# Optimization experiments

Measured on AMD Instinct MI355X. Metric: run time of the kernel, lower is better.

The kernel has to match this reference:

```python
import jax, jax.numpy as jnp
import numpy as np

H = 2048          # hidden_size
IM = 1024         # moe_intermediate_size
E = 16            # n_routed_experts
K = 8             # num_experts_per_tok
N_SHARED = 2      # n_shared_experts
IS = IM * N_SHARED  # shared expert intermediate
B, L = 1, 2048
SCALE = 2.5       # routed_scaling_factor
W_INIT = 0.02


def setup_inputs() -> dict:
    key = jax.random.key(0)
    ks = jax.random.split(key, 9)
    return {
        "hidden_states": jax.random.normal(ks[0], (B, L, H), jnp.float32),
        "gate_w": jax.random.normal(ks[1], (E, H), jnp.float32) * W_INIT,
        "Wg": jax.random.normal(ks[2], (E, H, IM), jnp.float32) * W_INIT,
        "Wu": jax.random.normal(ks[3], (E, H, IM), jnp.float32) * W_INIT,
        "Wd": jax.random.normal(ks[4], (E, IM, H), jnp.float32) * W_INIT,
        "sWg": jax.random.normal(ks[5], (H, IS), jnp.float32) * W_INIT,
        "sWu": jax.random.normal(ks[6], (H, IS), jnp.float32) * W_INIT,
        "sWd": jax.random.normal(ks[7], (IS, H), jnp.float32) * W_INIT,
    }


def reference(hidden_states, gate_w, Wg, Wu, Wd, sWg, sWu, sWd):
    orig_shape = hidden_states.shape
    h = hidden_states.reshape(-1, H)                      # [T, H]
    T = h.shape[0]

    # shared expert (SwiGLU MLP)
    shared = (jax.nn.silu(h @ sWg) * (h @ sWu)) @ sWd     # [T, H]

    # sigmoid router + top-k gating
    router_logits = h @ gate_w.T                          # [T, E]
    routing_weights = jax.nn.sigmoid(router_logits)
    topk_w, topk_idx = jax.lax.top_k(routing_weights, K)  # [T, K]
    topk_w = topk_w / (jnp.sum(topk_w, axis=-1, keepdims=True) + 1e-6)
    topk_w = topk_w * SCALE

    # dense [T, E] combine weights (zero for unselected experts)
    comb = jnp.zeros((T, E), h.dtype).at[jnp.arange(T)[:, None], topk_idx].add(topk_w)

    # all-expert SwiGLU MLP (batched over experts), then weighted combine
    g = jnp.einsum("th,ehi->eti", h, Wg)                  # [E, T, IM]
    u = jnp.einsum("th,ehi->eti", h, Wu)
    eo = jnp.einsum("eti,eih->eth", jax.nn.silu(g) * u, Wd)  # [E, T, H]
    routed = jnp.einsum("eth,te->th", eo, comb)           # [T, H]

    return (shared + routed).reshape(orig_shape)
```

## Files before the change

kernel.cpp:

```cpp
#include <hip/hip_runtime.h>
#include <hip/hip_bf16.h>
#include <stdint.h>

#define H_DIM  2048
#define IM_DIM 1024
#define E_NUM  16
#define TOPK   8
#define IS_DIM 2048
#define SCALE_F 2.5f

#define BM 128
#define BN 128
#define BK 32
#define LDSP 40

typedef __attribute__((ext_vector_type(8))) short   short8;
typedef __attribute__((ext_vector_type(8))) __bf16  bf16x8;
typedef __attribute__((ext_vector_type(4))) float   float4v;
typedef unsigned short ushort_t;

#define GLOAD_LDS16(gp, lp) \
    __builtin_amdgcn_global_load_lds((__attribute__((address_space(1))) void*)(gp), \
                                     (__attribute__((address_space(3))) void*)(lp), 16, 0, 0)

static __device__ __forceinline__ ushort_t f2bf(float x) {
    union { float f; uint32_t u; } v; v.f = x;
    uint32_t r = v.u + 0x7fffu + ((v.u >> 16) & 1u);
    return (ushort_t)(r >> 16);
}

__global__ void cast_h_kernel(const float* __restrict__ h, ushort_t* __restrict__ hb, int n4) {
    int i = blockIdx.x * blockDim.x + threadIdx.x;
    if (i < n4) {
        float4 v = ((const float4*)h)[i];
        ushort4 o;
        o.x = f2bf(v.x); o.y = f2bf(v.y); o.z = f2bf(v.z); o.w = f2bf(v.w);
        ((ushort4*)hb)[i] = o;
    }
}

__global__ void router_kernel(const float* __restrict__ h, const float* __restrict__ gw,
                              float* __restrict__ comb, int T) {
    int t = blockIdx.x;
    int l = threadIdx.x;
    const float* hr = h + (size_t)t * H_DIM;
    __shared__ float logits[E_NUM];
    for (int e = 0; e < E_NUM; e++) {
        const float* g = gw + e * H_DIM;
        float p = 0.f;
        #pragma unroll 8
        for (int j = l; j < H_DIM; j += 64) p += hr[j] * g[j];
        #pragma unroll
        for (int off = 32; off > 0; off >>= 1) p += __shfl_down(p, off);
        if (l == 0) logits[e] = p;
    }
    __syncthreads();
    if (l == 0) {
        float sig[E_NUM]; bool sel[E_NUM];
        #pragma unroll
        for (int e = 0; e < E_NUM; e++) { sig[e] = 1.f / (1.f + expf(-logits[e])); sel[e] = false; }
        #pragma unroll
        for (int k = 0; k < TOPK; k++) {
            int bi = 0; float bv = -1.f;
            #pragma unroll
            for (int e = 0; e < E_NUM; e++)
                if (!sel[e] && sig[e] > bv) { bv = sig[e]; bi = e; }
            sel[bi] = true;
        }
        float s = 0.f;
        #pragma unroll
        for (int e = 0; e < E_NUM; e++) if (sel[e]) s += sig[e];
        float inv = SCALE_F / (s + 1e-6f);
        #pragma unroll
        for (int e = 0; e < E_NUM; e++)
            comb[(size_t)t * E_NUM + e] = sel[e] ? sig[e] * inv : 0.f;
    }
}

__global__ __launch_bounds__(256)
void transpose_cvt_kernel(const float* __restrict__ src, ushort_t* __restrict__ dst,
                          int K, int N, size_t sStride, size_t dStride)
{
    __shared__ float tile[64 * 65];
    int z = blockIdx.z;
    const float* S = src + (size_t)z * sStride;
    ushort_t* D = dst + (size_t)z * dStride;
    int k0 = blockIdx.x * 64, n0 = blockIdx.y * 64;
    int tid = threadIdx.x;
    int tr = tid >> 4, tc = (tid & 15) * 4;
    #pragma unroll
    for (int p = 0; p < 4; p++) {
        int r = tr + 16 * p;
        float4 v = *(const float4*)&S[(size_t)(k0 + r) * N + n0 + tc];
        tile[(tc + 0) * 65 + r] = v.x;
        tile[(tc + 1) * 65 + r] = v.y;
        tile[(tc + 2) * 65 + r] = v.z;
        tile[(tc + 3) * 65 + r] = v.w;
    }
    __syncthreads();
    #pragma unroll
    for (int p = 0; p < 4; p++) {
        int n = tr + 16 * p;
        ushort4 o;
        o.x = f2bf(tile[n * 65 + tc + 0]);
        o.y = f2bf(tile[n * 65 + tc + 1]);
        o.z = f2bf(tile[n * 65 + tc + 2]);
        o.w = f2bf(tile[n * 65 + tc + 3]);
        *(ushort4*)&D[(size_t)(n0 + n) * K + k0 + tc] = o;
    }
}


__global__ __launch_bounds__(256, 2)
void gemm1f_kernel(const ushort_t* __restrict__ A, int lda,
                   const ushort_t* __restrict__ Bg0, const ushort_t* __restrict__ Bu0,
                   size_t bSeg,
                   ushort_t* __restrict__ C0, size_t cSeg, int ldc,
                   const float* __restrict__ comb, int Kdim)
{
    __shared__ ushort_t Als[BM * BK];
    __shared__ ushort_t Bgs[BN * BK];
    __shared__ ushort_t Bus[BN * BK];

    int z = blockIdx.z;
    const ushort_t* Bg = Bg0 + (size_t)z * bSeg;
    const ushort_t* Bu = Bu0 + (size_t)z * bSeg;
    ushort_t* C = C0 + (size_t)z * cSeg;
    int t0 = blockIdx.x * BM, n0 = blockIdx.y * BN;
    int tid = threadIdx.x, lane = tid & 63, wid = tid >> 6;
    int wm = (wid & 1) * 64, wn = (wid >> 1) * 64;
    int quad = lane >> 4, l15 = lane & 15;

    int srow = lane >> 2;
    int scol = (lane & 3) * 8;
    int rb = wid * 32;

    float4v accg[4][4], accu[4][4];
    #pragma unroll
    for (int i = 0; i < 4; i++)
        #pragma unroll
        for (int j = 0; j < 4; j++) {
            accg[i][j] = (float4v){0.f, 0.f, 0.f, 0.f};
            accu[i][j] = (float4v){0.f, 0.f, 0.f, 0.f};
        }

    const ushort_t* Ab0  = A  + (size_t)(t0 + rb + srow)      * lda  + scol;
    const ushort_t* Ab1  = A  + (size_t)(t0 + rb + 16 + srow) * lda  + scol;
    const ushort_t* Bgb0 = Bg + (size_t)(n0 + rb + srow)      * Kdim + scol;
    const ushort_t* Bgb1 = Bg + (size_t)(n0 + rb + 16 + srow) * Kdim + scol;
    const ushort_t* Bub0 = Bu + (size_t)(n0 + rb + srow)      * Kdim + scol;
    const ushort_t* Bub1 = Bu + (size_t)(n0 + rb + 16 + srow) * Kdim + scol;
    ushort_t* lA0  = &Als[rb * BK];
    ushort_t* lA1  = &Als[(rb + 16) * BK];
    ushort_t* lBg0 = &Bgs[rb * BK];
    ushort_t* lBg1 = &Bgs[(rb + 16) * BK];
    ushort_t* lBu0 = &Bus[rb * BK];
    ushort_t* lBu1 = &Bus[(rb + 16) * BK];

    for (int k0 = 0; k0 < Kdim; k0 += BK) {
        GLOAD_LDS16(Ab0 + k0,  lA0);
        GLOAD_LDS16(Ab1 + k0,  lA1);
        GLOAD_LDS16(Bgb0 + k0, lBg0);
        GLOAD_LDS16(Bgb1 + k0, lBg1);
        GLOAD_LDS16(Bub0 + k0, lBu0);
        GLOAD_LDS16(Bub1 + k0, lBu1);
        __syncthreads();

        bf16x8 af[4], bg[4], bu[4];
        #pragma unroll
        for (int i = 0; i < 4; i++)
            af[i] = *(const bf16x8*)&Als[(wm + i * 16 + l15) * BK + quad * 8];
        #pragma unroll
        for (int j = 0; j < 4; j++) {
            bg[j] = *(const bf16x8*)&Bgs[(wn + j * 16 + l15) * BK + quad * 8];
            bu[j] = *(const bf16x8*)&Bus[(wn + j * 16 + l15) * BK + quad * 8];
        }
        #pragma unroll
        for (int i = 0; i < 4; i++)
            #pragma unroll
            for (int j = 0; j < 4; j++) {
                accg[i][j] = __builtin_amdgcn_mfma_f32_16x16x32_bf16(af[i], bg[j], accg[i][j], 0, 0, 0);
                accu[i][j] = __builtin_amdgcn_mfma_f32_16x16x32_bf16(af[i], bu[j], accu[i][j], 0, 0, 0);
            }
        __syncthreads();
    }

    #pragma unroll
    for (int i = 0; i < 4; i++) {
        #pragma unroll
        for (int r = 0; r < 4; r++) {
            int t = t0 + wm + i * 16 + quad * 4 + r;
            float sc = comb ? comb[(size_t)t * E_NUM + z] : 1.f;
            #pragma unroll
            for (int j = 0; j < 4; j++) {
                float g = accg[i][j][r], u = accu[i][j][r];
                float sg = g / (1.f + __expf(-g));
                float v = sg * u * sc;
                int c = n0 + wn + j * 16 + l15;
                C[(size_t)t * ldc + c] = f2bf(v);
            }
        }
    }
}

__global__ __launch_bounds__(256, 2)
void gemm2f_kernel(const ushort_t* __restrict__ A0, size_t aSeg, int lda,
                   const ushort_t* __restrict__ B0, size_t bSeg,
                   float* __restrict__ Out, int N,
                   int nsegPerZ, int Kper, int mode)
{
    __shared__ ushort_t Als[BM * BK];
    __shared__ ushort_t Bls[BN * BK];

    int t0 = blockIdx.x * BM, n0 = blockIdx.y * BN;
    int z = blockIdx.z;
    int tid = threadIdx.x, lane = tid & 63, wid = tid >> 6;
    int wm = (wid & 1) * 64, wn = (wid >> 1) * 64;
    int quad = lane >> 4, l15 = lane & 15;

    int srow = lane >> 2;
    int scol = (lane & 3) * 8;
    int rb = wid * 32;

    float4v acc[4][4];
    #pragma unroll
    for (int i = 0; i < 4; i++)
        #pragma unroll
        for (int j = 0; j < 4; j++) acc[i][j] = (float4v){0.f, 0.f, 0.f, 0.f};

    ushort_t* lA0 = &Als[rb * BK];
    ushort_t* lA1 = &Als[(rb + 16) * BK];
    ushort_t* lB0 = &Bls[rb * BK];
    ushort_t* lB1 = &Bls[(rb + 16) * BK];

    for (int s = 0; s < nsegPerZ; s++) {
        int seg = z * nsegPerZ + s;
        const ushort_t* A = A0 + (size_t)seg * aSeg;
        const ushort_t* B = B0 + (size_t)seg * bSeg;
        const ushort_t* Ab0 = A + (size_t)(t0 + rb + srow)      * lda  + scol;
        const ushort_t* Ab1 = A + (size_t)(t0 + rb + 16 + srow) * lda  + scol;
        const ushort_t* Bb0 = B + (size_t)(n0 + rb + srow)      * Kper + scol;
        const ushort_t* Bb1 = B + (size_t)(n0 + rb + 16 + srow) * Kper + scol;

        for (int k0 = 0; k0 < Kper; k0 += BK) {
            GLOAD_LDS16(Ab0 + k0, lA0);
            GLOAD_LDS16(Ab1 + k0, lA1);
            GLOAD_LDS16(Bb0 + k0, lB0);
            GLOAD_LDS16(Bb1 + k0, lB1);
            __syncthreads();

            bf16x8 af[4], bf[4];
            #pragma unroll
            for (int i = 0; i < 4; i++)
                af[i] = *(const bf16x8*)&Als[(wm + i * 16 + l15) * BK + quad * 8];
            #pragma unroll
            for (int j = 0; j < 4; j++)
                bf[j] = *(const bf16x8*)&Bls[(wn + j * 16 + l15) * BK + quad * 8];
            #pragma unroll
            for (int i = 0; i < 4; i++)
                #pragma unroll
                for (int j = 0; j < 4; j++)
                    acc[i][j] = __builtin_amdgcn_mfma_f32_16x16x32_bf16(af[i], bf[j], acc[i][j], 0, 0, 0);
            __syncthreads();
        }
    }

    #pragma unroll
    for (int i = 0; i < 4; i++) {
        #pragma unroll
        for (int r = 0; r < 4; r++) {
            int t = t0 + wm + i * 16 + quad * 4 + r;
            #pragma unroll
            for (int j = 0; j < 4; j++) {
                int c = n0 + wn + j * 16 + l15;
                size_t idx = (size_t)t * N + c;
                float v = acc[i][j][r];
                if (mode == 0) Out[idx] = v;
                else if (mode == 1) Out[idx] += v;
                else atomicAdd(&Out[idx], v);
            }
        }
    }
}


__global__ __launch_bounds__(256)
void gemm1_kernel(const ushort_t* __restrict__ A, int lda,
                  const float* __restrict__ Bg0, const float* __restrict__ Bu0,
                  size_t bSeg, int ldb,
                  ushort_t* __restrict__ C0, size_t cSeg, int ldc,
                  const float* __restrict__ comb, int Kdim)
{
    __shared__ ushort_t Als[BM * LDSP];
    __shared__ ushort_t Bgs[BN * LDSP];
    __shared__ ushort_t Bus[BN * LDSP];

    int z = blockIdx.z;
    const float* Bg = Bg0 + (size_t)z * bSeg;
    const float* Bu = Bu0 + (size_t)z * bSeg;
    ushort_t* C = C0 + (size_t)z * cSeg;

    int t0 = blockIdx.x * BM;
    int n0 = blockIdx.y * BN;
    int tid = threadIdx.x;
    int lane = tid & 63, wid = tid >> 6;
    int wm = (wid & 1) * 64, wn = (wid >> 1) * 64;
    int quad = lane >> 4, l15 = lane & 15;

    float4v accg[4][4], accu[4][4];
    #pragma unroll
    for (int i = 0; i < 4; i++)
        #pragma unroll
        for (int j = 0; j < 4; j++) {
            accg[i][j] = (float4v){0.f, 0.f, 0.f, 0.f};
            accu[i][j] = (float4v){0.f, 0.f, 0.f, 0.f};
        }

    int a_r  = tid >> 2, a_oc = tid & 3;
    int b_ko = (tid >> 4) & 3;
    int b_n  = 2 * ((tid & 15) + ((tid >> 6) << 4));

    for (int k0 = 0; k0 < Kdim; k0 += BK) {
        __syncthreads();
        {
            const ushort_t* s0 = A + (size_t)(t0 + a_r) * lda + k0 + a_oc * 8;
            *(short8*)&Als[a_r * LDSP + a_oc * 8] = *(const short8*)s0;
            const ushort_t* s1 = A + (size_t)(t0 + a_r + 64) * lda + k0 + a_oc * 8;
            *(short8*)&Als[(a_r + 64) * LDSP + a_oc * 8] = *(const short8*)s1;
        }
        {
            short8 g0, g1, u0, u1;
            #pragma unroll
            for (int j = 0; j < 8; j++) {
                size_t roff = (size_t)(k0 + b_ko * 8 + j) * ldb + n0 + b_n;
                float2 vg = *(const float2*)&Bg[roff];
                float2 vu = *(const float2*)&Bu[roff];
                g0[j] = (short)f2bf(vg.x); g1[j] = (short)f2bf(vg.y);
                u0[j] = (short)f2bf(vu.x); u1[j] = (short)f2bf(vu.y);
            }
            *(short8*)&Bgs[b_n * LDSP + b_ko * 8]       = g0;
            *(short8*)&Bgs[(b_n + 1) * LDSP + b_ko * 8] = g1;
            *(short8*)&Bus[b_n * LDSP + b_ko * 8]       = u0;
            *(short8*)&Bus[(b_n + 1) * LDSP + b_ko * 8] = u1;
        }
        __syncthreads();

        bf16x8 af[4], bg[4], bu[4];
        #pragma unroll
        for (int i = 0; i < 4; i++)
            af[i] = *(const bf16x8*)&Als[(wm + i * 16 + l15) * LDSP + quad * 8];
        #pragma unroll
        for (int j = 0; j < 4; j++) {
            bg[j] = *(const bf16x8*)&Bgs[(wn + j * 16 + l15) * LDSP + quad * 8];
            bu[j] = *(const bf16x8*)&Bus[(wn + j * 16 + l15) * LDSP + quad * 8];
        }
        #pragma unroll
        for (int i = 0; i < 4; i++)
            #pragma unroll
            for (int j = 0; j < 4; j++) {
                accg[i][j] = __builtin_amdgcn_mfma_f32_16x16x32_bf16(af[i], bg[j], accg[i][j], 0, 0, 0);
                accu[i][j] = __builtin_amdgcn_mfma_f32_16x16x32_bf16(af[i], bu[j], accu[i][j], 0, 0, 0);
            }
    }

    #pragma unroll
// ... 31 lines not shown
    int quad = lane >> 4, l15 = lane & 15;

    float4v acc[4][4];
    #pragma unroll
    for (int i = 0; i < 4; i++)
        #pragma unroll
        for (int j = 0; j < 4; j++) acc[i][j] = (float4v){0.f, 0.f, 0.f, 0.f};

    int a_r  = tid >> 2, a_oc = tid & 3;
    int b_ko = (tid >> 4) & 3;
    int b_n  = 2 * ((tid & 15) + ((tid >> 6) << 4));

    for (int seg = 0; seg < nseg; seg++) {
        const ushort_t* A = A0 + (size_t)seg * aSeg;
        const float*    B = B0 + (size_t)seg * bSeg;
        for (int k0 = 0; k0 < Kper; k0 += BK) {
            __syncthreads();
            {
                const ushort_t* s0 = A + (size_t)(t0 + a_r) * lda + k0 + a_oc * 8;
                *(short8*)&Als[a_r * LDSP + a_oc * 8] = *(const short8*)s0;
                const ushort_t* s1 = A + (size_t)(t0 + a_r + 64) * lda + k0 + a_oc * 8;
                *(short8*)&Als[(a_r + 64) * LDSP + a_oc * 8] = *(const short8*)s1;
            }
            {
                short8 r0, r1;
                #pragma unroll
                for (int j = 0; j < 8; j++) {
                    size_t roff = (size_t)(k0 + b_ko * 8 + j) * ldb + n0 + b_n;
                    float2 v = *(const float2*)&B[roff];
                    r0[j] = (short)f2bf(v.x); r1[j] = (short)f2bf(v.y);
                }
                *(short8*)&Bls[b_n * LDSP + b_ko * 8]       = r0;
                *(short8*)&Bls[(b_n + 1) * LDSP + b_ko * 8] = r1;
            }
            __syncthreads();

            bf16x8 af[4], bf[4];
            #pragma unroll
            for (int i = 0; i < 4; i++)
                af[i] = *(const bf16x8*)&Als[(wm + i * 16 + l15) * LDSP + quad * 8];
            #pragma unroll
            for (int j = 0; j < 4; j++)
                bf[j] = *(const bf16x8*)&Bls[(wn + j * 16 + l15) * LDSP + quad * 8];
            #pragma unroll
            for (int i = 0; i < 4; i++)
                #pragma unroll
                for (int j = 0; j < 4; j++)
                    acc[i][j] = __builtin_amdgcn_mfma_f32_16x16x32_bf16(af[i], bf[j], acc[i][j], 0, 0, 0);
        }
    }

    #pragma unroll
    for (int i = 0; i < 4; i++) {
        #pragma unroll
        for (int r = 0; r < 4; r++) {
            int t = t0 + wm + i * 16 + quad * 4 + r;
            #pragma unroll
            for (int j = 0; j < 4; j++) {
                int c = n0 + wn + j * 16 + l15;
                size_t idx = (size_t)t * N + c;
                float v = acc[i][j][r];
                if (accum) Out[idx] += v; else Out[idx] = v;
            }
        }
    }
}


extern "C" void kernel_launch(void* const* d_in, const int* in_sizes, int n_in,
                              void* d_out, int out_size, void* d_ws, size_t ws_size,
                              hipStream_t stream) {
    const float* h      = (const float*)d_in[0];
    const float* gate_w = (const float*)d_in[1];
    const float* Wg     = (const float*)d_in[2];
    const float* Wu     = (const float*)d_in[3];
    const float* Wd     = (const float*)d_in[4];
    const float* sWg    = (const float*)d_in[5];
    const float* sWu    = (const float*)d_in[6];
    const float* sWd    = (const float*)d_in[7];
    float* out = (float*)d_out;
    int T = in_sizes[0] / H_DIM;
    (void)n_in; (void)out_size;

    char* ws = (char*)d_ws;
    size_t off = 0;
    auto alloc = [&](size_t bytes) -> void* {
        void* p = ws + off;
        off = (off + bytes + 255) & ~(size_t)255;
        return p;
    };
    ushort_t* h_bf  = (ushort_t*)alloc((size_t)T * H_DIM * 2);
    float*    comb  = (float*)   alloc((size_t)T * E_NUM * 4);
    ushort_t* act_s = (ushort_t*)alloc((size_t)T * IS_DIM * 2);
    ushort_t* act_r = (ushort_t*)alloc((size_t)E_NUM * T * IM_DIM * 2);
    ushort_t* bufS1 = (ushort_t*)alloc((size_t)IS_DIM * H_DIM * 2);
    ushort_t* bufS2 = (ushort_t*)alloc((size_t)IS_DIM * H_DIM * 2);
    ushort_t* bufW1 = (ushort_t*)alloc((size_t)E_NUM * IM_DIM * H_DIM * 2);
    ushort_t* bufW2 = (ushort_t*)alloc((size_t)E_NUM * IM_DIM * H_DIM * 2);
    size_t need = off;

    int n4 = T * H_DIM / 4;
    cast_h_kernel<<<(n4 + 255) / 256, 256, 0, stream>>>(h, h_bf, n4);
    router_kernel<<<T, 64, 0, stream>>>(h, gate_w, comb, T);

    if (ws_size >= need) {
        transpose_cvt_kernel<<<dim3(H_DIM / 64, IS_DIM / 64, 1), 256, 0, stream>>>(
            sWg, bufS1, H_DIM, IS_DIM, 0, 0);
        transpose_cvt_kernel<<<dim3(H_DIM / 64, IS_DIM / 64, 1), 256, 0, stream>>>(
            sWu, bufS2, H_DIM, IS_DIM, 0, 0);
        gemm1f_kernel<<<dim3(T / BM, IS_DIM / BN, 1), 256, 0, stream>>>(
            h_bf, H_DIM, bufS1, bufS2, 0, act_s, 0, IS_DIM, nullptr, H_DIM);

        transpose_cvt_kernel<<<dim3(H_DIM / 64, IM_DIM / 64, E_NUM), 256, 0, stream>>>(
            Wg, bufW1, H_DIM, IM_DIM, (size_t)H_DIM * IM_DIM, (size_t)IM_DIM * H_DIM);
        transpose_cvt_kernel<<<dim3(H_DIM / 64, IM_DIM / 64, E_NUM), 256, 0, stream>>>(
            Wu, bufW2, H_DIM, IM_DIM, (size_t)H_DIM * IM_DIM, (size_t)IM_DIM * H_DIM);
        gemm1f_kernel<<<dim3(T / BM, IM_DIM / BN, E_NUM), 256, 0, stream>>>(
            h_bf, H_DIM, bufW1, bufW2, (size_t)IM_DIM * H_DIM,
            act_r, (size_t)T * IM_DIM, IM_DIM, comb, H_DIM);

        transpose_cvt_kernel<<<dim3(IS_DIM / 64, H_DIM / 64, 1), 256, 0, stream>>>(
            sWd, bufS1, IS_DIM, H_DIM, 0, 0);
        gemm2f_kernel<<<dim3(T / BM, H_DIM / BN, 1), 256, 0, stream>>>(
            act_s, 0, IS_DIM, bufS1, 0, out, H_DIM, 1, IS_DIM, 0);

        transpose_cvt_kernel<<<dim3(IM_DIM / 64, H_DIM / 64, E_NUM), 256, 0, stream>>>(
            Wd, bufW1, IM_DIM, H_DIM, (size_t)IM_DIM * H_DIM, (size_t)H_DIM * IM_DIM);
        gemm2f_kernel<<<dim3(T / BM, H_DIM / BN, 2), 256, 0, stream>>>(
            act_r, (size_t)T * IM_DIM, IM_DIM, bufW1, (size_t)H_DIM * IM_DIM,
            out, H_DIM, E_NUM / 2, IM_DIM, 2);
    } else {
        gemm1_kernel<<<dim3(T / BM, IS_DIM / BN, 1), 256, 0, stream>>>(
            h_bf, H_DIM, sWg, sWu, 0, IS_DIM, act_s, 0, IS_DIM, nullptr, H_DIM);
        gemm1_kernel<<<dim3(T / BM, IM_DIM / BN, E_NUM), 256, 0, stream>>>(
            h_bf, H_DIM, Wg, Wu, (size_t)H_DIM * IM_DIM, IM_DIM,
            act_r, (size_t)T * IM_DIM, IM_DIM, comb, H_DIM);
        gemm2_kernel<<<dim3(T / BM, H_DIM / BN, 1), 256, 0, stream>>>(
            act_s, 0, IS_DIM, sWd, 0, H_DIM, out, H_DIM, 1, IS_DIM, 0);
        gemm2_kernel<<<dim3(T / BM, H_DIM / BN, 1), 256, 0, stream>>>(
            act_r, (size_t)T * IM_DIM, IM_DIM, Wd, (size_t)IM_DIM * H_DIM, H_DIM,
            out, H_DIM, E_NUM, IM_DIM, 1);
    }
}
```

Measured before the change: 1.147 ms.

## Rewrite expert GEMMs as double-buffered 512-thread kernels with shared experts as extra segments

Replaces the single-buffered 128x128 GEMM kernels with 256x128-tile, 512-thread kernels. They use double-buffered LDS with a 64-wide K step, XOR-swizzled LDS layout, explicit vmcnt waits and raised MFMA priority, so global loads overlap with compute. The shared expert is split into two IM-wide segments and appended to the routed experts, so one batched launch per GEMM stage covers all 18 segments. The down projection splits segments across 6 z-slices that atomically accumulate into an output zeroed up front. This trades more fp32 atomics and a larger LDS footprint (one block per CU) for fewer launches and better latency hiding.

```diff
diff --git a/kernel.cpp b/kernel.cpp
--- a/kernel.cpp
+++ b/kernel.cpp
@@ -23,10 +23,18 @@
     __builtin_amdgcn_global_load_lds((__attribute__((address_space(1))) void*)(gp), \
                                      (__attribute__((address_space(3))) void*)(lp), 16, 0, 0)
 
+#define BAR()    asm volatile("s_barrier" ::: "memory")
+#define VMCNT(n) asm volatile("s_waitcnt vmcnt(" #n ")" ::: "memory")
+
 static __device__ __forceinline__ ushort_t f2bf(float x) {
     union { float f; uint32_t u; } v; v.f = x;
     uint32_t r = v.u + 0x7fffu + ((v.u >> 16) & 1u);
     return (ushort_t)(r >> 16);
+}
+
+__global__ void zero4_kernel(float4* __restrict__ p, int n4) {
+    int i = blockIdx.x * blockDim.x + threadIdx.x;
+    if (i < n4) p[i] = make_float4(0.f, 0.f, 0.f, 0.f);
 }
 
 __global__ void cast_h_kernel(const float* __restrict__ h, ushort_t* __restrict__ hb, int n4) {
@@ -111,176 +119,280 @@
 }
 
 
-__global__ __launch_bounds__(256, 2)
-void gemm1f_kernel(const ushort_t* __restrict__ A, int lda,
-                   const ushort_t* __restrict__ Bg0, const ushort_t* __restrict__ Bu0,
-                   size_t bSeg,
-                   ushort_t* __restrict__ C0, size_t cSeg, int ldc,
-                   const float* __restrict__ comb, int Kdim)
+__global__ __launch_bounds__(512, 1)
+void gemm1_8p(const ushort_t* __restrict__ A,
+              const ushort_t* __restrict__ G0,
+              const ushort_t* __restrict__ U0,
+              ushort_t* __restrict__ C0,
+              const float* __restrict__ comb, int T)
 {
-    __shared__ ushort_t Als[BM * BK];
-    __shared__ ushort_t Bgs[BN * BK];
-    __shared__ ushort_t Bus[BN * BK];
-
-    int z = blockIdx.z;
-    const ushort_t* Bg = Bg0 + (size_t)z * bSeg;
-    const ushort_t* Bu = Bu0 + (size_t)z * bSeg;
-    ushort_t* C = C0 + (size_t)z * cSeg;
-    int t0 = blockIdx.x * BM, n0 = blockIdx.y * BN;
-    int tid = threadIdx.x, lane = tid & 63, wid = tid >> 6;
-    int wm = (wid & 1) * 64, wn = (wid >> 1) * 64;
-    int quad = lane >> 4, l15 = lane & 15;
-
-    int srow = lane >> 2;
-    int scol = (lane & 3) * 8;
-    int rb = wid * 32;
-
-    float4v accg[4][4], accu[4][4];
-    #pragma unroll
-    for (int i = 0; i < 4; i++)
-        #pragma unroll
-        for (int j = 0; j < 4; j++) {
+    __shared__ ushort_t As[2][256 * 64];
+    __shared__ ushort_t Gs[2][128 * 64];
+    __shared__ ushort_t Us[2][128 * 64];
+
+    const int z   = blockIdx.z;
+    const int t0  = blockIdx.x * 256;
+    const int n0  = blockIdx.y * 128;
+    const int tid = threadIdx.x;
+    const int lane = tid & 63, wid = tid >> 6;
+    const int wm = (wid >> 2) * 128;
+    const int wn = (wid & 3) * 32;
+    const int quad = lane >> 4, l15 = lane & 15;
+    const int sw = l15 & 7;
+
+    const int lrow8 = lane >> 3;
+    const int lslot = (lane & 7) ^ lrow8;
+
+    const ushort_t* G = G0 + (size_t)z * IM_DIM * H_DIM;
+    const ushort_t* U = U0 + (size_t)z * IM_DIM * H_DIM;
+    ushort_t*       C = C0 + (size_t)z * T * IM_DIM;
+
+    const int aq0 = wm + (wid & 3) * 32;
+    const int bq0 = (wid & 3) * 32 + (wid >> 2) * 16;
+    const ushort_t* aG = A + (size_t)(t0 + aq0 + lrow8) * H_DIM + lslot * 8;
+    const ushort_t* gG = G + (size_t)(n0 + bq0 + lrow8) * H_DIM + lslot * 8;
+    const ushort_t* uG = U + (size_t)(n0 + bq0 + lrow8) * H_DIM + lslot * 8;
+
+#define G1_ISSUE_A(bb, ko) do { \
+    GLOAD_LDS16(aG + (ko),               &As[bb][(aq0 + 0) * 64]);  \
+    GLOAD_LDS16(aG + (ko) + 8 * H_DIM,   &As[bb][(aq0 + 8) * 64]);  \
+    GLOAD_LDS16(aG + (ko) + 16 * H_DIM,  &As[bb][(aq0 + 16) * 64]); \
+    GLOAD_LDS16(aG + (ko) + 24 * H_DIM,  &As[bb][(aq0 + 24) * 64]); \
+} while (0)
+#define G1_ISSUE_G(bb, ko) do { \
+    GLOAD_LDS16(gG + (ko),               &Gs[bb][(bq0 + 0) * 64]);  \
+    GLOAD_LDS16(gG + (ko) + 8 * H_DIM,   &Gs[bb][(bq0 + 8) * 64]);  \
+} while (0)
+#define G1_ISSUE_U(bb, ko) do { \
+    GLOAD_LDS16(uG + (ko),               &Us[bb][(bq0 + 0) * 64]);  \
+    GLOAD_LDS16(uG + (ko) + 8 * H_DIM,   &Us[bb][(bq0 + 8) * 64]);  \
+} while (0)
+
+    float4v accg[8][2], accu[8][2];
+    #pragma unroll
+    for (int i = 0; i < 8; ++i)
+        #pragma unroll
+        for (int j = 0; j < 2; ++j) {
             accg[i][j] = (float4v){0.f, 0.f, 0.f, 0.f};
             accu[i][j] = (float4v){0.f, 0.f, 0.f, 0.f};
         }
 
-    const ushort_t* Ab0  = A  + (size_t)(t0 + rb + srow)      * lda  + scol;
-    const ushort_t* Ab1  = A  + (size_t)(t0 + rb + 16 + srow) * lda  + scol;
-    const ushort_t* Bgb0 = Bg + (size_t)(n0 + rb + srow)      * Kdim + scol;
-    const ushort_t* Bgb1 = Bg + (size_t)(n0 + rb + 16 + srow) * Kdim + scol;
-    const ushort_t* Bub0 = Bu + (size_t)(n0 + rb + srow)      * Kdim + scol;
-    const ushort_t* Bub1 = Bu + (size_t)(n0 + rb + 16 + srow) * Kdim + scol;
-    ushort_t* lA0  = &Als[rb * BK];
-    ushort_t* lA1  = &Als[(rb + 16) * BK];
-    ushort_t* lBg0 = &Bgs[rb * BK];
-    ushort_t* lBg1 = &Bgs[(rb + 16) * BK];
-    ushort_t* lBu0 = &Bus[rb * BK];
-    ushort_t* lBu1 = &Bus[(rb + 16) * BK];
-
-    for (int k0 = 0; k0 < Kdim; k0 += BK) {
-        GLOAD_LDS16(Ab0 + k0,  lA0);
-        GLOAD_LDS16(Ab1 + k0,  lA1);
-        GLOAD_LDS16(Bgb0 + k0, lBg0);
-        GLOAD_LDS16(Bgb1 + k0, lBg1);
-        GLOAD_LDS16(Bub0 + k0, lBu0);
-        GLOAD_LDS16(Bub1 + k0, lBu1);
-        __syncthreads();
-
-        bf16x8 af[4], bg[4], bu[4];
-        #pragma unroll
-        for (int i = 0; i < 4; i++)
-            af[i] = *(const bf16x8*)&Als[(wm + i * 16 + l15) * BK + quad * 8];
-        #pragma unroll
-        for (int j = 0; j < 4; j++) {
-            bg[j] = *(const bf16x8*)&Bgs[(wn + j * 16 + l15) * BK + quad * 8];
-            bu[j] = *(const bf16x8*)&Bus[(wn + j * 16 + l15) * BK + quad * 8];
-        }
-        #pragma unroll
-        for (int i = 0; i < 4; i++)
-            #pragma unroll
-            for (int j = 0; j < 4; j++) {
-                accg[i][j] = __builtin_amdgcn_mfma_f32_16x16x32_bf16(af[i], bg[j], accg[i][j], 0, 0, 0);
-                accu[i][j] = __builtin_amdgcn_mfma_f32_16x16x32_bf16(af[i], bu[j], accu[i][j], 0, 0, 0);
+    G1_ISSUE_A(0, 0); G1_ISSUE_G(0, 0); G1_ISSUE_U(0, 0);
+
+    const int NT = H_DIM / 64;
+    for (int t = 0; t < NT; ++t) {
+        const int b  = t & 1;
+        const int ko = (t + 1) * 64;
+        if (t + 1 < NT) {
+            G1_ISSUE_A(b ^ 1, ko);
+            G1_ISSUE_G(b ^ 1, ko);
+            VMCNT(6);
+        } else {
+            VMCNT(0);
+        }
+        BAR();
+
+        bf16x8 a_[4][2], g_[2][2], u_[2][2];
+        #pragma unroll
+        for (int i = 0; i < 4; ++i) {
+            const int r = wm + i * 16 + l15;
+            #pragma unroll
+            for (int kk = 0; kk < 2; ++kk)
+                a_[i][kk] = *(const bf16x8*)&As[b][r * 64 + (((kk * 4 + quad) ^ sw) << 3)];
+        }
+        #pragma unroll
+        for (int j = 0; j < 2; ++j) {
+            const int r = wn + j * 16 + l15;
+            #pragma unroll
+            for (int kk = 0; kk < 2; ++kk)
+                g_[j][kk] = *(const bf16x8*)&Gs[b][r * 64 + (((kk * 4 + quad) ^ sw) << 3)];
+        }
+        __builtin_amdgcn_s_setprio(1);
+        #pragma unroll
+        for (int i = 0; i < 4; ++i)
+            #pragma unroll
+            for (int j = 0; j < 2; ++j)
+                #pragma unroll
+                for (int kk = 0; kk < 2; ++kk)
+                    accg[i][j] = __builtin_amdgcn_mfma_f32_16x16x32_bf16(a_[i][kk], g_[j][kk], accg[i][j], 0, 0, 0);
+        __builtin_amdgcn_s_setprio(0);
+        BAR();
+
+        if (t + 1 < NT) G1_ISSUE_U(b ^ 1, ko);
+        #pragma unroll
+        for (int j = 0; j < 2; ++j) {
+            const int r = wn + j * 16 + l15;
+            #pragma unroll
+            for (int kk = 0; kk < 2; ++kk)
+                u_[j][kk] = *(const bf16x8*)&Us[b][r * 64 + (((kk * 4 + quad) ^ sw) << 3)];
+        }
+        __builtin_amdgcn_s_setprio(1);
+        #pragma unroll
+        for (int i = 0; i < 4; ++i)
+            #pragma unroll
+            for (int j = 0; j < 2; ++j)
+                #pragma unroll
+                for (int kk = 0; kk < 2; ++kk)
+                    accu[i][j] = __builtin_amdgcn_mfma_f32_16x16x32_bf16(a_[i][kk], u_[j][kk], accu[i][j], 0, 0, 0);
+        __builtin_amdgcn_s_setprio(0);
+        BAR();
+
+        #pragma unroll
+        for (int i = 0; i < 4; ++i) {
+            const int r = wm + (i + 4) * 16 + l15;
+            #pragma unroll
+            for (int kk = 0; kk < 2; ++kk)
+                a_[i][kk] = *(const bf16x8*)&As[b][r * 64 + (((kk * 4 + quad) ^ sw) << 3)];
+        }
+        __builtin_amdgcn_s_setprio(1);
+        #pragma unroll
+        for (int i = 0; i < 4; ++i)
+            #pragma unroll
+            for (int j = 0; j < 2; ++j)
+                #pragma unroll
+                for (int kk = 0; kk < 2; ++kk)
+                    accg[i + 4][j] = __builtin_amdgcn_mfma_f32_16x16x32_bf16(a_[i][kk], g_[j][kk], accg[i + 4][j], 0, 0, 0);
+        __builtin_amdgcn_s_setprio(0);
+        BAR();
+
+        __builtin_amdgcn_s_setprio(1);
+        #pragma unroll
+        for (int i = 0; i < 4; ++i)
+            #pragma unroll
+            for (int j = 0; j < 2; ++j)
+                #pragma unroll
+                for (int kk = 0; kk < 2; ++kk)
+                    accu[i + 4][j] = __builtin_amdgcn_mfma_f32_16x16x32_bf16(a_[i][kk], u_[j][kk], accu[i + 4][j], 0, 0, 0);
+        __builtin_amdgcn_s_setprio(0);
+    }
+
+    #pragma unroll
+    for (int i = 0; i < 8; ++i) {
+        #pragma unroll
+        for (int r = 0; r < 4; ++r) {
+            const int tr = t0 + wm + i * 16 + quad * 4 + r;
+            const float sc = (z < E_NUM) ? comb[(size_t)tr * E_NUM + z] : 1.f;
+            #pragma unroll
+            for (int j = 0; j < 2; ++j) {
+                const float g = accg[i][j][r], u = accu[i][j][r];
+                const float v = (g / (1.f + __expf(-g))) * u * sc;
+                C[(size_t)tr * IM_DIM + (n0 + wn + j * 16 + l15)] = f2bf(v);
             }
-        __syncthreads();
-    }
-
-    #pragma unroll
-    for (int i = 0; i < 4; i++) {
-        #pragma unroll
-        for (int r = 0; r < 4; r++) {
-            int t = t0 + wm + i * 16 + quad * 4 + r;
-            float sc = comb ? comb[(size_t)t * E_NUM + z] : 1.f;
-            #pragma unroll
-            for (int j = 0; j < 4; j++) {
-                float g = accg[i][j][r], u = accu[i][j][r];
-                float sg = g / (1.f + __expf(-g));
-                float v = sg * u * sc;
-                int c = n0 + wn + j * 16 + l15;
-                C[(size_t)t * ldc + c] = f2bf(v);
-            }
-        }
-    }
-}
-
-__global__ __launch_bounds__(256, 2)
-void gemm2f_kernel(const ushort_t* __restrict__ A0, size_t aSeg, int lda,
-                   const ushort_t* __restrict__ B0, size_t bSeg,
-                   float* __restrict__ Out, int N,
-                   int nsegPerZ, int Kper, int mode)
+        }
+    }
+#undef G1_ISSUE_A
+#undef G1_ISSUE_G
+#undef G1_ISSUE_U
+}
+
+__global__ __launch_bounds__(512, 1)
+void gemm2_8p(const ushort_t* __restrict__ A0,
+              const ushort_t* __restrict__ B0,
+              float* __restrict__ Out, int T, int nseg)
 {
-    __shared__ ushort_t Als[BM * BK];
-    __shared__ ushort_t Bls[BN * BK];
-
-    int t0 = blockIdx.x * BM, n0 = blockIdx.y * BN;
-    int z = blockIdx.z;
-    int tid = threadIdx.x, lane = tid & 63, wid = tid >> 6;
-    int wm = (wid & 1) * 64, wn = (wid >> 1) * 64;
-    int quad = lane >> 4, l15 = lane & 15;
-
-    int srow = lane >> 2;
-    int scol = (lane & 3) * 8;
-    int rb = wid * 32;
+    __shared__ ushort_t As[2][256 * 64];
+    __shared__ ushort_t Bs[2][128 * 64];
+
+    const int z   = blockIdx.z;
+    const int t0  = blockIdx.x * 256;
+    const int n0  = blockIdx.y * 128;
+    const int tid = threadIdx.x;
+    const int lane = tid & 63, wid = tid >> 6;
+    const int wm = (wid >> 1) * 64;
+    const int wn = (wid & 1) * 64;
+    const int quad = lane >> 4, l15 = lane & 15;
+    const int sw = l15 & 7;
+    const int lrow8 = lane >> 3;
+    const int lslot = (lane & 7) ^ lrow8;
+
+    const int aq0 = (wid >> 1) * 64 + (wid & 1) * 32;
+    const int bq0 = (wid & 1) * 64 + (wid >> 1) * 16;
+    const ushort_t* aG = A0 + (size_t)(t0 + aq0 + lrow8) * IM_DIM + lslot * 8;
+    const ushort_t* bG = B0 + (size_t)(n0 + bq0 + lrow8) * IM_DIM + lslot * 8;
+    const size_t segA = (size_t)T * IM_DIM;
+    const size_t segB = (size_t)H_DIM * IM_DIM;
+
+#define G2_ISSUE(bb, tt) do { \
+    const int    s_  = z * nseg + ((tt) >> 4); \
+    const size_t ao_ = (size_t)s_ * segA + ((tt) & 15) * 64; \
+    const size_t bo_ = (size_t)s_ * segB + ((tt) & 15) * 64; \
+    GLOAD_LDS16(aG + ao_,                &As[bb][(aq0 + 0) * 64]);  \
+    GLOAD_LDS16(aG + ao_ + 8 * IM_DIM,   &As[bb][(aq0 + 8) * 64]);  \
+    GLOAD_LDS16(aG + ao_ + 16 * IM_DIM,  &As[bb][(aq0 + 16) * 64]); \
+    GLOAD_LDS16(aG + ao_ + 24 * IM_DIM,  &As[bb][(aq0 + 24) * 64]); \
+    GLOAD_LDS16(bG + bo_,                &Bs[bb][(bq0 + 0) * 64]);  \
+    GLOAD_LDS16(bG + bo_ + 8 * IM_DIM,   &Bs[bb][(bq0 + 8) * 64]);  \
+} while (0)
 
     float4v acc[4][4];
     #pragma unroll
-    for (int i = 0; i < 4; i++)
-        #pragma unroll
-        for (int j = 0; j < 4; j++) acc[i][j] = (float4v){0.f, 0.f, 0.f, 0.f};
-
-    ushort_t* lA0 = &Als[rb * BK];
-    ushort_t* lA1 = &Als[(rb + 16) * BK];
-    ushort_t* lB0 = &Bls[rb * BK];
-    ushort_t* lB1 = &Bls[(rb + 16) * BK];
-
-    for (int s = 0; s < nsegPerZ; s++) {
-        int seg = z * nsegPerZ + s;
-        const ushort_t* A = A0 + (size_t)seg * aSeg;
-        const ushort_t* B = B0 + (size_t)seg * bSeg;
-        const ushort_t* Ab0 = A + (size_t)(t0 + rb + srow)      * lda  + scol;
-        const ushort_t* Ab1 = A + (size_t)(t0 + rb + 16 + srow) * lda  + scol;
-        const ushort_t* Bb0 = B + (size_t)(n0 + rb + srow)      * Kper + scol;
-        const ushort_t* Bb1 = B + (size_t)(n0 + rb + 16 + srow) * Kper + scol;
-
-        for (int k0 = 0; k0 < Kper; k0 += BK) {
-            GLOAD_LDS16(Ab0 + k0, lA0);
-            GLOAD_LDS16(Ab1 + k0, lA1);
-            GLOAD_LDS16(Bb0 + k0, lB0);
-            GLOAD_LDS16(Bb1 + k0, lB1);
-            __syncthreads();
-
-            bf16x8 af[4], bf[4];
-            #pragma unroll
-            for (int i = 0; i < 4; i++)
-                af[i] = *(const bf16x8*)&Als[(wm + i * 16 + l15) * BK + quad * 8];
-            #pragma unroll
-            for (int j = 0; j < 4; j++)
-                bf[j] = *(const bf16x8*)&Bls[(wn + j * 16 + l15) * BK + quad * 8];
-            #pragma unroll
-            for (int i = 0; i < 4; i++)
-                #pragma unroll
-                for (int j = 0; j < 4; j++)
-                    acc[i][j] = __builtin_amdgcn_mfma_f32_16x16x32_bf16(af[i], bf[j], acc[i][j], 0, 0, 0);
-            __syncthreads();
-        }
-    }
-
-    #pragma unroll
-    for (int i = 0; i < 4; i++) {
-        #pragma unroll
-        for (int r = 0; r < 4; r++) {
-            int t = t0 + wm + i * 16 + quad * 4 + r;
-            #pragma unroll
-            for (int j = 0; j < 4; j++) {
-                int c = n0 + wn + j * 16 + l15;
-                size_t idx = (size_t)t * N + c;
-                float v = acc[i][j][r];
-                if (mode == 0) Out[idx] = v;
-                else if (mode == 1) Out[idx] += v;
-                else atomicAdd(&Out[idx], v);
-            }
-        }
-    }
+    for (int i = 0; i < 4; ++i)
+        #pragma unroll
+        for (int j = 0; j < 4; ++j) acc[i][j] = (float4v){0.f, 0.f, 0.f, 0.f};
+
+    G2_ISSUE(0, 0);
+    const int nTT = nseg * (IM_DIM / 64);
+    for (int tt = 0; tt < nTT; ++tt) {
+        const int b = tt & 1;
+        if (tt + 1 < nTT) { G2_ISSUE(b ^ 1, tt + 1); VMCNT(6); }
+        else              { VMCNT(0); }
+        BAR();
+
+        bf16x8 a_[4][2], b_[4][2];
+        #pragma unroll
+        for (int i = 0; i < 4; ++i) {
+            const int r = wm + i * 16 + l15;
+            #pragma unroll
+            for (int kk = 0; kk < 2; ++kk)
+                a_[i][kk] = *(const bf16x8*)&As[b][r * 64 + (((kk * 4 + quad) ^ sw) << 3)];
+        }
+        #pragma unroll
+        for (int j = 0; j < 2; ++j) {
+            const int r = wn + j * 16 + l15;
+            #pragma unroll
+            for (int kk = 0; kk < 2; ++kk)
+                b_[j][kk] = *(const bf16x8*)&Bs[b][r * 64 + (((kk * 4 + quad) ^ sw) << 3)];
+        }
+        __builtin_amdgcn_s_setprio(1);
+        #pragma unroll
+        for (int i = 0; i < 4; ++i)
+            #pragma unroll
+            for (int j = 0; j < 2; ++j)
+                #pragma unroll
+                for (int kk = 0; kk < 2; ++kk)
+                    acc[i][j] = __builtin_amdgcn_mfma_f32_16x16x32_bf16(a_[i][kk], b_[j][kk], acc[i][j], 0, 0, 0);
+        __builtin_amdgcn_s_setprio(0);
+        BAR();
+
+        #pragma unroll
+        for (int j = 0; j < 2; ++j) {
+            const int r = wn + (j + 2) * 16 + l15;
+            #pragma unroll
+            for (int kk = 0; kk < 2; ++kk)
+                b_[j + 2][kk] = *(const bf16x8*)&Bs[b][r * 64 + (((kk * 4 + quad) ^ sw) << 3)];
+        }
+        __builtin_amdgcn_s_setprio(1);
+        #pragma unroll
+        for (int i = 0; i < 4; ++i)
+            #pragma unroll
+            for (int j = 2; j < 4; ++j)
+                #pragma unroll
+                for (int kk = 0; kk < 2; ++kk)
+                    acc[i][j] = __builtin_amdgcn_mfma_f32_16x16x32_bf16(a_[i][kk], b_[j][kk], acc[i][j], 0, 0, 0);
+        __builtin_amdgcn_s_setprio(0);
+        BAR();
+    }
+
+    #pragma unroll
+    for (int i = 0; i < 4; ++i)
+        #pragma unroll
+        for (int r = 0; r < 4; ++r) {
+            const int tr = t0 + wm + i * 16 + quad * 4 + r;
+            #pragma unroll
+            for (int j = 0; j < 4; ++j)
+                atomicAdd(&Out[(size_t)tr * H_DIM + n0 + wn + j * 16 + l15], acc[i][j][r]);
+        }
+#undef G2_ISSUE
 }
 
 
@@ -478,6 +590,8 @@
     int T = in_sizes[0] / H_DIM;
     (void)n_in; (void)out_size;
 
+    const int NSEG = E_NUM + 2;
+
     char* ws = (char*)d_ws;
     size_t off = 0;
     auto alloc = [&](size_t bytes) -> void* {
@@ -485,14 +599,11 @@
         off = (off + bytes + 255) & ~(size_t)255;
         return p;
     };
-    ushort_t* h_bf  = (ushort_t*)alloc((size_t)T * H_DIM * 2);
-    float*    comb  = (float*)   alloc((size_t)T * E_NUM * 4);
-    ushort_t* act_s = (ushort_t*)alloc((size_t)T * IS_DIM * 2);
-    ushort_t* act_r = (ushort_t*)alloc((size_t)E_NUM * T * IM_DIM * 2);
-    ushort_t* bufS1 = (ushort_t*)alloc((size_t)IS_DIM * H_DIM * 2);
-    ushort_t* bufS2 = (ushort_t*)alloc((size_t)IS_DIM * H_DIM * 2);
-    ushort_t* bufW1 = (ushort_t*)alloc((size_t)E_NUM * IM_DIM * H_DIM * 2);
-    ushort_t* bufW2 = (ushort_t*)alloc((size_t)E_NUM * IM_DIM * H_DIM * 2);
+    ushort_t* h_bf = (ushort_t*)alloc((size_t)T * H_DIM * 2);
+    float*    comb = (float*)   alloc((size_t)T * E_NUM * 4);
+    ushort_t* act  = (ushort_t*)alloc((size_t)NSEG * T * IM_DIM * 2);
+    ushort_t* bufG = (ushort_t*)alloc((size_t)NSEG * IM_DIM * H_DIM * 2);
+    ushort_t* bufU = (ushort_t*)alloc((size_t)NSEG * IM_DIM * H_DIM * 2);
     size_t need = off;
 
     int n4 = T * H_DIM / 4;
@@ -500,32 +611,33 @@
     router_kernel<<<T, 64, 0, stream>>>(h, gate_w, comb, T);
 
     if (ws_size >= need) {
-        transpose_cvt_kernel<<<dim3(H_DIM / 64, IS_DIM / 64, 1), 256, 0, stream>>>(
-            sWg, bufS1, H_DIM, IS_DIM, 0, 0);
-        transpose_cvt_kernel<<<dim3(H_DIM / 64, IS_DIM / 64, 1), 256, 0, stream>>>(
-            sWu, bufS2, H_DIM, IS_DIM, 0, 0);
-        gemm1f_kernel<<<dim3(T / BM, IS_DIM / BN, 1), 256, 0, stream>>>(
-            h_bf, H_DIM, bufS1, bufS2, 0, act_s, 0, IS_DIM, nullptr, H_DIM);
+        zero4_kernel<<<(n4 + 255) / 256, 256, 0, stream>>>((float4*)out, n4);
 
         transpose_cvt_kernel<<<dim3(H_DIM / 64, IM_DIM / 64, E_NUM), 256, 0, stream>>>(
-            Wg, bufW1, H_DIM, IM_DIM, (size_t)H_DIM * IM_DIM, (size_t)IM_DIM * H_DIM);
+            Wg, bufG, H_DIM, IM_DIM, (size_t)H_DIM * IM_DIM, (size_t)IM_DIM * H_DIM);
+        transpose_cvt_kernel<<<dim3(H_DIM / 64, IM_DIM / 64, 2), 256, 0, stream>>>(
+            sWg, bufG + (size_t)E_NUM * IM_DIM * H_DIM, H_DIM, IS_DIM,
+            (size_t)IM_DIM, (size_t)IM_DIM * H_DIM);
         transpose_cvt_kernel<<<dim3(H_DIM / 64, IM_DIM / 64, E_NUM), 256, 0, stream>>>(
-            Wu, bufW2, H_DIM, IM_DIM, (size_t)H_DIM * IM_DIM, (size_t)IM_DIM * H_DIM);
-        gemm1f_kernel<<<dim3(T / BM, IM_DIM / BN, E_NUM), 256, 0, stream>>>(
-            h_bf, H_DIM, bufW1, bufW2, (size_t)IM_DIM * H_DIM,
-            act_r, (size_t)T * IM_DIM, IM_DIM, comb, H_DIM);
-
-        transpose_cvt_kernel<<<dim3(IS_DIM / 64, H_DIM / 64, 1), 256, 0, stream>>>(
-            sWd, bufS1, IS_DIM, H_DIM, 0, 0);
-        gemm2f_kernel<<<dim3(T / BM, H_DIM / BN, 1), 256, 0, stream>>>(
-            act_s, 0, IS_DIM, bufS1, 0, out, H_DIM, 1, IS_DIM, 0);
+            Wu, bufU, H_DIM, IM_DIM, (size_t)H_DIM * IM_DIM, (size_t)IM_DIM * H_DIM);
+        transpose_cvt_kernel<<<dim3(H_DIM / 64, IM_DIM / 64, 2), 256, 0, stream>>>(
+            sWu, bufU + (size_t)E_NUM * IM_DIM * H_DIM, H_DIM, IS_DIM,
+            (size_t)IM_DIM, (size_t)IM_DIM * H_DIM);
+
+        gemm1_8p<<<dim3(T / 256, IM_DIM / 128, NSEG), 512, 0, stream>>>(
+            h_bf, bufG, bufU, act, comb, T);
 
         transpose_cvt_kernel<<<dim3(IM_DIM / 64, H_DIM / 64, E_NUM), 256, 0, stream>>>(
-            Wd, bufW1, IM_DIM, H_DIM, (size_t)IM_DIM * H_DIM, (size_t)H_DIM * IM_DIM);
-        gemm2f_kernel<<<dim3(T / BM, H_DIM / BN, 2), 256, 0, stream>>>(
-            act_r, (size_t)T * IM_DIM, IM_DIM, bufW1, (size_t)H_DIM * IM_DIM,
-            out, H_DIM, E_NUM / 2, IM_DIM, 2);
+            Wd, bufG, IM_DIM, H_DIM, (size_t)IM_DIM * H_DIM, (size_t)H_DIM * IM_DIM);
+        transpose_cvt_kernel<<<dim3(IM_DIM / 64, H_DIM / 64, 2), 256, 0, stream>>>(
+            sWd, bufG + (size_t)E_NUM * H_DIM * IM_DIM, IM_DIM, H_DIM,
+            (size_t)IM_DIM * H_DIM, (size_t)H_DIM * IM_DIM);
+
+        gemm2_8p<<<dim3(T / 256, H_DIM / 128, 6), 512, 0, stream>>>(
+            act, bufG, out, T, 3);
     } else {
+        ushort_t* act_r = act;
+        ushort_t* act_s = act + (size_t)E_NUM * T * IM_DIM;
         gemm1_kernel<<<dim3(T / BM, IS_DIM / BN, 1), 256, 0, stream>>>(
             h_bf, H_DIM, sWg, sWu, 0, IS_DIM, act_s, 0, IS_DIM, nullptr, H_DIM);
         gemm1_kernel<<<dim3(T / BM, IM_DIM / BN, E_NUM), 256, 0, stream>>>(
```

New measurement: 1.205 ms. +5.1%, slower.

## Compute routed experts only on their routed tokens via gather/scatter grouped GEMMs

Applied to the files above, without the earlier changes.

The router now builds per-expert token lists and weights with atomic counters. The routed gate/up GEMM gathers only each expert's selected token rows, and the down GEMM scatters results back with atomicAdd, replacing dense all-expert computation. With top-8 of 16 experts this is meant to cut routed FLOPs roughly in half. The cost is non-deterministic token ordering, more atomic output traffic, and early-exit blocks whose count depends on routing balance.

```diff
diff --git a/kernel.cpp b/kernel.cpp
--- a/kernel.cpp
+++ b/kernel.cpp
@@ -27,6 +27,11 @@
     union { float f; uint32_t u; } v; v.f = x;
     uint32_t r = v.u + 0x7fffu + ((v.u >> 16) & 1u);
     return (ushort_t)(r >> 16);
+}
+
+__global__ void zero4_kernel(float4* __restrict__ p, int n4) {
+    int i = blockIdx.x * blockDim.x + threadIdx.x;
+    if (i < n4) p[i] = make_float4(0.f, 0.f, 0.f, 0.f);
 }
 
 __global__ void cast_h_kernel(const float* __restrict__ h, ushort_t* __restrict__ hb, int n4) {
@@ -40,7 +45,9 @@
 }
 
 __global__ void router_kernel(const float* __restrict__ h, const float* __restrict__ gw,
-                              float* __restrict__ comb, int T) {
+                              float* __restrict__ comb,
+                              int* __restrict__ cnt, int* __restrict__ tlist,
+                              float* __restrict__ wlist, int T) {
     int t = blockIdx.x;
     int l = threadIdx.x;
     const float* hr = h + (size_t)t * H_DIM;
@@ -72,8 +79,15 @@
         for (int e = 0; e < E_NUM; e++) if (sel[e]) s += sig[e];
         float inv = SCALE_F / (s + 1e-6f);
         #pragma unroll
-        for (int e = 0; e < E_NUM; e++)
-            comb[(size_t)t * E_NUM + e] = sel[e] ? sig[e] * inv : 0.f;
+        for (int e = 0; e < E_NUM; e++) {
+            float w = sel[e] ? sig[e] * inv : 0.f;
+            comb[(size_t)t * E_NUM + e] = w;
+            if (sel[e]) {
+                int pos = atomicAdd(&cnt[e], 1);
+                tlist[(size_t)e * T + pos] = t;
+                wlist[(size_t)e * T + pos] = w;
+            }
+        }
     }
 }
 
@@ -204,6 +218,110 @@
 }
 
 __global__ __launch_bounds__(256, 2)
+void gemm1g_kernel(const ushort_t* __restrict__ A,
+                   const ushort_t* __restrict__ Bg0,
+                   const ushort_t* __restrict__ Bu0,
+                   ushort_t* __restrict__ C0,
+                   const int* __restrict__ cnt,
+                   const int* __restrict__ tlist,
+                   const float* __restrict__ wlist, int T)
+{
+    __shared__ ushort_t Als[BM * BK];
+    __shared__ ushort_t Bgs[BN * BK];
+    __shared__ ushort_t Bus[BN * BK];
+
+    int z = blockIdx.z;
+    int cn = cnt[z];
+    int t0 = blockIdx.x * BM;
+    if (t0 >= cn) return;
+
+    const ushort_t* Bg = Bg0 + (size_t)z * IM_DIM * H_DIM;
+    const ushort_t* Bu = Bu0 + (size_t)z * IM_DIM * H_DIM;
+    ushort_t* C = C0 + (size_t)z * T * IM_DIM;
+    const int* tl = tlist + (size_t)z * T;
+    int n0 = blockIdx.y * BN;
+    int tid = threadIdx.x, lane = tid & 63, wid = tid >> 6;
+    int wm = (wid & 1) * 64, wn = (wid >> 1) * 64;
+    int quad = lane >> 4, l15 = lane & 15;
+
+    int srow = lane >> 2;
+    int scol = (lane & 3) * 8;
+    int rb = wid * 32;
+
+    float4v accg[4][4], accu[4][4];
+    #pragma unroll
+    for (int i = 0; i < 4; i++)
+        #pragma unroll
+        for (int j = 0; j < 4; j++) {
+            accg[i][j] = (float4v){0.f, 0.f, 0.f, 0.f};
+            accu[i][j] = (float4v){0.f, 0.f, 0.f, 0.f};
+        }
+
+    int p0 = t0 + rb + srow, p1 = p0 + 16;
+    int r0 = tl[p0 < cn ? p0 : cn - 1];
+    int r1 = tl[p1 < cn ? p1 : cn - 1];
+    const ushort_t* Ab0  = A  + (size_t)r0 * H_DIM + scol;
+    const ushort_t* Ab1  = A  + (size_t)r1 * H_DIM + scol;
+    const ushort_t* Bgb0 = Bg + (size_t)(n0 + rb + srow)      * H_DIM + scol;
+    const ushort_t* Bgb1 = Bg + (size_t)(n0 + rb + 16 + srow) * H_DIM + scol;
+    const ushort_t* Bub0 = Bu + (size_t)(n0 + rb + srow)      * H_DIM + scol;
+    const ushort_t* Bub1 = Bu + (size_t)(n0 + rb + 16 + srow) * H_DIM + scol;
+    ushort_t* lA0  = &Als[rb * BK];
+    ushort_t* lA1  = &Als[(rb + 16) * BK];
+    ushort_t* lBg0 = &Bgs[rb * BK];
+    ushort_t* lBg1 = &Bgs[(rb + 16) * BK];
+    ushort_t* lBu0 = &Bus[rb * BK];
+    ushort_t* lBu1 = &Bus[(rb + 16) * BK];
+
+    for (int k0 = 0; k0 < H_DIM; k0 += BK) {
+        GLOAD_LDS16(Ab0 + k0,  lA0);
+        GLOAD_LDS16(Ab1 + k0,  lA1);
+        GLOAD_LDS16(Bgb0 + k0, lBg0);
+        GLOAD_LDS16(Bgb1 + k0, lBg1);
+        GLOAD_LDS16(Bub0 + k0, lBu0);
+        GLOAD_LDS16(Bub1 + k0, lBu1);
+        __syncthreads();
+
+        bf16x8 af[4], bg[4], bu[4];
+        #pragma unroll
+        for (int i = 0; i < 4; i++)
+            af[i] = *(const bf16x8*)&Als[(wm + i * 16 + l15) * BK + quad * 8];
+        #pragma unroll
+        for (int j = 0; j < 4; j++) {
+            bg[j] = *(const bf16x8*)&Bgs[(wn + j * 16 + l15) * BK + quad * 8];
+            bu[j] = *(const bf16x8*)&Bus[(wn + j * 16 + l15) * BK + quad * 8];
+        }
+        #pragma unroll
+        for (int i = 0; i < 4; i++)
+            #pragma unroll
+            for (int j = 0; j < 4; j++) {
+                accg[i][j] = __builtin_amdgcn_mfma_f32_16x16x32_bf16(af[i], bg[j], accg[i][j], 0, 0, 0);
+                accu[i][j] = __builtin_amdgcn_mfma_f32_16x16x32_bf16(af[i], bu[j], accu[i][j], 0, 0, 0);
+            }
+        __syncthreads();
+    }
+
+    #pragma unroll
+    for (int i = 0; i < 4; i++) {
+        #pragma unroll
+        for (int r = 0; r < 4; r++) {
+            int pos = t0 + wm + i * 16 + quad * 4 + r;
+            if (pos < cn) {
+                float sc = wlist[(size_t)z * T + pos];
+                #pragma unroll
+                for (int j = 0; j < 4; j++) {
+                    float g = accg[i][j][r], u = accu[i][j][r];
+                    float sg = g / (1.f + __expf(-g));
+                    float v = sg * u * sc;
+                    int c = n0 + wn + j * 16 + l15;
+                    C[(size_t)pos * IM_DIM + c] = f2bf(v);
+                }
+            }
+        }
+    }
+}
+
+__global__ __launch_bounds__(256, 2)
 void gemm2f_kernel(const ushort_t* __restrict__ A0, size_t aSeg, int lda,
                    const ushort_t* __restrict__ B0, size_t bSeg,
                    float* __restrict__ Out, int N,
@@ -278,6 +396,87 @@
                 if (mode == 0) Out[idx] = v;
                 else if (mode == 1) Out[idx] += v;
                 else atomicAdd(&Out[idx], v);
+            }
+        }
+    }
+}
+
+__global__ __launch_bounds__(256, 2)
+void gemm2g_kernel(const ushort_t* __restrict__ A0,
+                   const ushort_t* __restrict__ B0,
+                   float* __restrict__ Out,
+                   const int* __restrict__ cnt,
+                   const int* __restrict__ tlist, int T)
+{
+    __shared__ ushort_t Als[BM * BK];
+    __shared__ ushort_t Bls[BN * BK];
+
+    int z = blockIdx.z;
+    int cn = cnt[z];
+    int t0 = blockIdx.x * BM;
+    if (t0 >= cn) return;
+
+    const ushort_t* A = A0 + (size_t)z * T * IM_DIM;
+    const ushort_t* B = B0 + (size_t)z * H_DIM * IM_DIM;
+    const int* tl = tlist + (size_t)z * T;
+    int n0 = blockIdx.y * BN;
+    int tid = threadIdx.x, lane = tid & 63, wid = tid >> 6;
+    int wm = (wid & 1) * 64, wn = (wid >> 1) * 64;
+    int quad = lane >> 4, l15 = lane & 15;
+
+    int srow = lane >> 2;
+    int scol = (lane & 3) * 8;
+    int rb = wid * 32;
+
+    float4v acc[4][4];
+    #pragma unroll
+    for (int i = 0; i < 4; i++)
+        #pragma unroll
+        for (int j = 0; j < 4; j++) acc[i][j] = (float4v){0.f, 0.f, 0.f, 0.f};
+
+    const ushort_t* Ab0 = A + (size_t)(t0 + rb + srow)      * IM_DIM + scol;
+    const ushort_t* Ab1 = A + (size_t)(t0 + rb + 16 + srow) * IM_DIM + scol;
+    const ushort_t* Bb0 = B + (size_t)(n0 + rb + srow)      * IM_DIM + scol;
+    const ushort_t* Bb1 = B + (size_t)(n0 + rb + 16 + srow) * IM_DIM + scol;
+    ushort_t* lA0 = &Als[rb * BK];
+    ushort_t* lA1 = &Als[(rb + 16) * BK];
+    ushort_t* lB0 = &Bls[rb * BK];
+    ushort_t* lB1 = &Bls[(rb + 16) * BK];
+
+    for (int k0 = 0; k0 < IM_DIM; k0 += BK) {
+        GLOAD_LDS16(Ab0 + k0, lA0);
+        GLOAD_LDS16(Ab1 + k0, lA1);
+        GLOAD_LDS16(Bb0 + k0, lB0);
+        GLOAD_LDS16(Bb1 + k0, lB1);
+        __syncthreads();
+
+        bf16x8 af[4], bf[4];
+        #pragma unroll
+        for (int i = 0; i < 4; i++)
+            af[i] = *(const bf16x8*)&Als[(wm + i * 16 + l15) * BK + quad * 8];
+        #pragma unroll
+        for (int j = 0; j < 4; j++)
+            bf[j] = *(const bf16x8*)&Bls[(wn + j * 16 + l15) * BK + quad * 8];
+        #pragma unroll
+        for (int i = 0; i < 4; i++)
+            #pragma unroll
+            for (int j = 0; j < 4; j++)
+                acc[i][j] = __builtin_amdgcn_mfma_f32_16x16x32_bf16(af[i], bf[j], acc[i][j], 0, 0, 0);
+        __syncthreads();
+    }
+
+    #pragma unroll
+    for (int i = 0; i < 4; i++) {
+        #pragma unroll
+        for (int r = 0; r < 4; r++) {
+            int pos = t0 + wm + i * 16 + quad * 4 + r;
+            if (pos < cn) {
+                int tok = tl[pos];
+                #pragma unroll
+                for (int j = 0; j < 4; j++) {
+                    int c = n0 + wn + j * 16 + l15;
+                    atomicAdd(&Out[(size_t)tok * H_DIM + c], acc[i][j][r]);
+                }
             }
         }
     }
@@ -487,6 +686,9 @@
     };
     ushort_t* h_bf  = (ushort_t*)alloc((size_t)T * H_DIM * 2);
     float*    comb  = (float*)   alloc((size_t)T * E_NUM * 4);
+    int*      cnt   = (int*)     alloc((size_t)E_NUM * 4);
+    int*      tlist = (int*)     alloc((size_t)E_NUM * T * 4);
+    float*    wlist = (float*)   alloc((size_t)E_NUM * T * 4);
     ushort_t* act_s = (ushort_t*)alloc((size_t)T * IS_DIM * 2);
     ushort_t* act_r = (ushort_t*)alloc((size_t)E_NUM * T * IM_DIM * 2);
     ushort_t* bufS1 = (ushort_t*)alloc((size_t)IS_DIM * H_DIM * 2);
@@ -497,7 +699,8 @@
 
     int n4 = T * H_DIM / 4;
     cast_h_kernel<<<(n4 + 255) / 256, 256, 0, stream>>>(h, h_bf, n4);
-    router_kernel<<<T, 64, 0, stream>>>(h, gate_w, comb, T);
+    zero4_kernel<<<1, 64, 0, stream>>>((float4*)cnt, E_NUM * 4 / 16);
+    router_kernel<<<T, 64, 0, stream>>>(h, gate_w, comb, cnt, tlist, wlist, T);
 
     if (ws_size >= need) {
         transpose_cvt_kernel<<<dim3(H_DIM / 64, IS_DIM / 64, 1), 256, 0, stream>>>(
@@ -511,9 +714,8 @@
             Wg, bufW1, H_DIM, IM_DIM, (size_t)H_DIM * IM_DIM, (size_t)IM_DIM * H_DIM);
         transpose_cvt_kernel<<<dim3(H_DIM / 64, IM_DIM / 64, E_NUM), 256, 0, stream>>>(
             Wu, bufW2, H_DIM, IM_DIM, (size_t)H_DIM * IM_DIM, (size_t)IM_DIM * H_DIM);
-        gemm1f_kernel<<<dim3(T / BM, IM_DIM / BN, E_NUM), 256, 0, stream>>>(
-            h_bf, H_DIM, bufW1, bufW2, (size_t)IM_DIM * H_DIM,
-            act_r, (size_t)T * IM_DIM, IM_DIM, comb, H_DIM);
+        gemm1g_kernel<<<dim3(T / BM, IM_DIM / BN, E_NUM), 256, 0, stream>>>(
+            h_bf, bufW1, bufW2, act_r, cnt, tlist, wlist, T);
 
         transpose_cvt_kernel<<<dim3(IS_DIM / 64, H_DIM / 64, 1), 256, 0, stream>>>(
             sWd, bufS1, IS_DIM, H_DIM, 0, 0);
@@ -522,9 +724,8 @@
 
         transpose_cvt_kernel<<<dim3(IM_DIM / 64, H_DIM / 64, E_NUM), 256, 0, stream>>>(
             Wd, bufW1, IM_DIM, H_DIM, (size_t)IM_DIM * H_DIM, (size_t)H_DIM * IM_DIM);
-        gemm2f_kernel<<<dim3(T / BM, H_DIM / BN, 2), 256, 0, stream>>>(
-            act_r, (size_t)T * IM_DIM, IM_DIM, bufW1, (size_t)H_DIM * IM_DIM,
-            out, H_DIM, E_NUM / 2, IM_DIM, 2);
+        gemm2g_kernel<<<dim3(T / BM, H_DIM / BN, E_NUM), 256, 0, stream>>>(
+            act_r, bufW1, out, cnt, tlist, T);
     } else {
         gemm1_kernel<<<dim3(T / BM, IS_DIM / BN, 1), 256, 0, stream>>>(
             h_bf, H_DIM, sWg, sWu, 0, IS_DIM, act_s, 0, IS_DIM, nullptr, H_DIM);
```

New measurement: 1.283 ms. 1.12x slower.
